# Kernel tuning notes

Measured on AMD Instinct MI355X. Metric: run time of the kernel, lower is better.

## Reference

```python
import jax, jax.numpy as jnp
import numpy as np

N, E, D_IN, D, L = 50000, 800000, 128, 256, 3
BN_EPS = 1e-5


def _bn(x, gamma, beta):
    # torch BatchNorm1d training-mode forward: biased batch statistics over node dim
    m = x.mean(axis=0)
    v = x.var(axis=0)  # ddof=0, matches torch normalization
    return gamma * (x - m) * jax.lax.rsqrt(v + BN_EPS) + beta


def setup_inputs() -> dict:
    key = jax.random.key(0)
    ks = jax.random.split(key, 12)
    s_in = 1.0 / np.sqrt(D_IN)
    s_d = 1.0 / np.sqrt(D)
    s_2d = 1.0 / np.sqrt(2 * D)
    return {
        "pre_node_emb": jax.random.normal(ks[0], (1, N, D_IN), jnp.float32),
        "edge_index": jax.random.randint(ks[1], (1, E, 2), 0, N, jnp.int64),
        "W0": jax.random.uniform(ks[2], (D_IN, D), jnp.float32, -s_in, s_in),
        "b0": jax.random.uniform(ks[3], (D,), jnp.float32, -s_in, s_in),
        "W1": jax.random.uniform(ks[4], (L, D, 2 * D), jnp.float32, -s_d, s_d),
        "b1": jax.random.uniform(ks[5], (L, 2 * D), jnp.float32, -s_d, s_d),
        "g1": jnp.ones((L, 2 * D), jnp.float32),
        "beta1": jnp.zeros((L, 2 * D), jnp.float32),
        "W2": jax.random.uniform(ks[6], (L, 2 * D, D), jnp.float32, -s_2d, s_2d),
        "b2": jax.random.uniform(ks[7], (L, D), jnp.float32, -s_2d, s_2d),
        "gf": jnp.ones((L, D), jnp.float32),
        "betaf": jnp.zeros((L, D), jnp.float32),
    }


def reference(pre_node_emb, edge_index, W0, b0, W1, b1, g1, beta1, W2, b2, gf, betaf):
    x = pre_node_emb[0]            # [N, D_IN]
    ei = edge_index[0]             # [E, 2] -> transposed in torch; rows are (src, dst)
    src, dst = ei[:, 0], ei[:, 1]
    x = x @ W0 + b0                # node embedder -> [N, D]
    for l in range(L):
        # GINConv (eps=0): sum-aggregate neighbor messages, then MLP
        agg = jax.ops.segment_sum(x[src], dst, num_segments=N)   # scatter-add
        h = x + agg
        h = h @ W1[l] + b1[l]
        h = _bn(h, g1[l], beta1[l])
        h = jax.nn.relu(h)
        h = h @ W2[l] + b2[l]
        x = _bn(h + x, gf[l], betaf[l])  # residual + outer BatchNorm
    return x
```

## Files before the change

kernel.cpp:

```cpp
#include <hip/hip_runtime.h>

#define MNODES 50000
#define M_PAD  50048
#define NEDGES 800000
#define DIN    128
#define DD     256
#define D2     512
#define NLAYERS 3
#define BN_EPS 1e-5f
#define NREP   16

typedef unsigned short ushort_t;
typedef __bf16 v8bf __attribute__((ext_vector_type(8)));
typedef unsigned short v8us __attribute__((ext_vector_type(8)));
typedef float  v4f  __attribute__((ext_vector_type(4)));

#define GLOBAL_AS __attribute__((address_space(1)))
#define LDS_AS    __attribute__((address_space(3)))

__device__ __forceinline__ float bf2f(ushort_t u) {
    unsigned x = ((unsigned)u) << 16;
    return __uint_as_float(x);
}
__device__ __forceinline__ ushort_t f2bf(float f) {
    unsigned u = __float_as_uint(f);
    u += 0x7FFF + ((u >> 16) & 1);
    return (ushort_t)(u >> 16);
}
__device__ __forceinline__ void async16(const ushort_t* g, ushort_t* l) {
    __builtin_amdgcn_global_load_lds((const GLOBAL_AS unsigned int*)g,
                                     (LDS_AS unsigned int*)l, 16, 0, 0);
}
#define BARRIER() asm volatile("s_barrier" ::: "memory")
#define VMWAIT8() asm volatile("s_waitcnt vmcnt(8)" ::: "memory")
#define VMWAIT4() asm volatile("s_waitcnt vmcnt(4)" ::: "memory")
#define VMWAIT0() asm volatile("s_waitcnt vmcnt(0)" ::: "memory")
#define LGKM0()   asm volatile("s_waitcnt lgkmcnt(0)" ::: "memory")

#define R0 (M_PAD * DIN)
#define R0V (R0 / 4)
#define RW (DIN * DD + 2 * NLAYERS * DD * D2)
#define NSTATZ (NREP * D2 * 2 + NREP * DD * 2)
__global__ void k_prep_all(const float* __restrict__ pre, ushort_t* __restrict__ preb,
                           const float* __restrict__ W0, const float* __restrict__ W1,
                           const float* __restrict__ W2,
                           ushort_t* __restrict__ W0T, ushort_t* __restrict__ W1T,
                           ushort_t* __restrict__ W2T,
                           float* __restrict__ caf, float* __restrict__ ccf,
                           float* __restrict__ statz, int* __restrict__ deg) {
    int i = blockIdx.x * blockDim.x + threadIdx.x;
    if (i < R0V) {
        int row = i >> 5;
        ushort4 o;
        if (row < MNODES) {
            float4 v = ((const float4*)pre)[i];
            o.x = f2bf(v.x); o.y = f2bf(v.y); o.z = f2bf(v.z); o.w = f2bf(v.w);
        } else {
            o.x = 0; o.y = 0; o.z = 0; o.w = 0;
        }
        ((ushort4*)preb)[i] = o;
        return;
    }
    int j = i - R0V;
    if (j < RW) {
        if (j < DIN * DD) {
            int n = j >> 7, k = j & 127;
            W0T[j] = f2bf(W0[k * DD + n]);
        } else if (j < DIN * DD + NLAYERS * DD * D2) {
            int j2 = j - DIN * DD;
            int l = j2 >> 17, off = j2 & 131071;
            int n = off >> 8, k = off & 255;
            W1T[(size_t)l * 131072 + off] = f2bf(W1[(size_t)l * 131072 + k * D2 + n]);
        } else {
            int j2 = j - DIN * DD - NLAYERS * DD * D2;
            int l = j2 >> 17, off = j2 & 131071;
            int n = off >> 9, k = off & 511;
            W2T[(size_t)l * 131072 + off] = f2bf(W2[(size_t)l * 131072 + k * DD + n]);
        }
        return;
    }
    j -= RW;
    if (j < 256) { caf[j] = 1.f; ccf[j] = 0.f; return; }
    j -= 256;
    if (j < NSTATZ) { statz[j] = 0.f; return; }
    j -= NSTATZ;
    if (j < MNODES) deg[j] = 0;
}

__global__ void k_hist(const int* __restrict__ ei, int* __restrict__ deg) {
    int e = blockIdx.x * blockDim.x + threadIdx.x;
    if (e < NEDGES) atomicAdd(&deg[ei[e * 2 + 1]], 1);
}
__global__ void k_scan1(const int* __restrict__ deg, int* __restrict__ rowptr,
                        int* __restrict__ bsum, int n) {
    __shared__ int tmp[256];
    int tid = threadIdx.x;
    int i = blockIdx.x * 256 + tid;
    int v = (i < n) ? deg[i] : 0;
    tmp[tid] = v;
    __syncthreads();
    #pragma unroll
    for (int off = 1; off < 256; off <<= 1) {
        int t = (tid >= off) ? tmp[tid - off] : 0;
        __syncthreads();
        tmp[tid] += t;
        __syncthreads();
    }
    if (i < n) rowptr[i + 1] = tmp[tid];
    if (tid == 255) bsum[blockIdx.x] = tmp[255];
}
__global__ __launch_bounds__(256)
void k_scan2(int* __restrict__ bsum, int nb) {
    __shared__ int tmp[256];
    int tid = threadIdx.x;
    int v = (tid < nb) ? bsum[tid] : 0;
    tmp[tid] = v;
    __syncthreads();
    #pragma unroll
    for (int off = 1; off < 256; off <<= 1) {
        int t = (tid >= off) ? tmp[tid - off] : 0;
        __syncthreads();
        tmp[tid] += t;
        __syncthreads();
    }
    if (tid < nb) bsum[tid] = tmp[tid] - v;
}
__global__ void k_scan3(const int* __restrict__ deg, const int* __restrict__ bsum,
                        int* __restrict__ rowptr, int* __restrict__ cursor, int n) {
    int i = blockIdx.x * 256 + threadIdx.x;
    if (i == 0) rowptr[0] = 0;
    if (i < n) {
        int incl = rowptr[i + 1] + bsum[i >> 8];
        rowptr[i + 1] = incl;
        cursor[i] = incl - deg[i];
    }
}
__global__ void k_fill(const int* __restrict__ ei, int* __restrict__ cursor,
                       int* __restrict__ col) {
    int e = blockIdx.x * blockDim.x + threadIdx.x;
    if (e < NEDGES) {
        int pos = atomicAdd(&cursor[ei[e * 2 + 1]], 1);
        col[pos] = ei[e * 2];
    }
}

__global__ void k_gather(const int* __restrict__ rowptr, const int* __restrict__ col,
                         const ushort_t* __restrict__ x, const float* __restrict__ ca,
                         const float* __restrict__ cc, ushort_t* __restrict__ out) {
    int node = blockIdx.x * 4 + (threadIdx.x >> 6);
    int lane = threadIdx.x & 63;
    if (node >= MNODES) return;
    const ushort4* xp = (const ushort4*)x;
    ushort4 v = xp[(size_t)node * 64 + lane];
    float a0 = bf2f(v.x), a1 = bf2f(v.y), a2 = bf2f(v.z), a3 = bf2f(v.w);
    int s = rowptr[node], e = rowptr[node + 1];
    int i = s;
    for (; i + 7 < e; i += 8) {
        ushort4 u[8];
        #pragma unroll
        for (int j = 0; j < 8; j++) u[j] = xp[(size_t)col[i + j] * 64 + lane];
        #pragma unroll
        for (int j = 0; j < 8; j++) {
            a0 += bf2f(u[j].x); a1 += bf2f(u[j].y);
            a2 += bf2f(u[j].z); a3 += bf2f(u[j].w);
        }
    }
    for (; i < e; i++) {
        ushort4 u = xp[(size_t)col[i] * 64 + lane];
        a0 += bf2f(u.x); a1 += bf2f(u.y); a2 += bf2f(u.z); a3 += bf2f(u.w);
    }
    int c = lane * 4;
    float dn = (float)(e - s) + 1.0f;
    ushort4 o;
    o.x = f2bf(ca[c + 0] * a0 + dn * cc[c + 0]);
    o.y = f2bf(ca[c + 1] * a1 + dn * cc[c + 1]);
    o.z = f2bf(ca[c + 2] * a2 + dn * cc[c + 2]);
    o.w = f2bf(ca[c + 3] * a3 + dn * cc[c + 3]);
    ((ushort4*)out)[(size_t)node * 64 + lane] = o;
}

__global__ void k_coeffs(float* __restrict__ sums, float* __restrict__ sumsq,
                         const float* __restrict__ g, const float* __restrict__ beta,
                         float* __restrict__ ca, float* __restrict__ cc,
                         float2* __restrict__ cacc, int n) {
    int c = blockIdx.x * blockDim.x + threadIdx.x;
    if (c >= n) return;
    float s = 0.f, q = 0.f;
    #pragma unroll
    for (int r = 0; r < NREP; r++) {
        s += sums[r * n + c];  sums[r * n + c]  = 0.f;
        q += sumsq[r * n + c]; sumsq[r * n + c] = 0.f;
    }
    float mean = s * (1.0f / MNODES);
    float var  = q * (1.0f / MNODES) - mean * mean;
    float a    = g[c] * rsqrtf(var + BN_EPS);
    float b    = beta[c] - a * mean;
    ca[c] = a;
    cc[c] = b;
    if (cacc) cacc[c] = make_float2(a, b);
}

__global__ void k_apply_out(const ushort_t* __restrict__ h, const float* __restrict__ ca,
                            const float* __restrict__ cc, float* __restrict__ out) {
    int i = blockIdx.x * blockDim.x + threadIdx.x;
    if (i >= MNODES * 64) return;
    int c = (i & 63) * 4;
    ushort4 v = ((const ushort4*)h)[i];
    float4 o;
    o.x = ca[c + 0] * bf2f(v.x) + cc[c + 0];
    o.y = ca[c + 1] * bf2f(v.y) + cc[c + 1];
    o.z = ca[c + 2] * bf2f(v.z) + cc[c + 2];
    o.w = ca[c + 3] * bf2f(v.w) + cc[c + 3];
    ((float4*)out)[i] = o;
}

#define LOADA(buf, st)                                                        \
    { buf[0] = *(const v8bf*)(Ap + (st) * 32);                                \
      buf[1] = *(const v8bf*)(Ap + 16 * KT + (st) * 32); }

template<int DO_STATS, int RES, int FUSE_BN, int KT>
__global__ __launch_bounds__(256, 3)
void k_gemm_bf(const ushort_t* __restrict__ A, const ushort_t* __restrict__ WT,
               const float* __restrict__ bias,
               const ushort_t* resid, const float* __restrict__ r_ca,
               const float* __restrict__ r_cc, const float2* __restrict__ cacc,
               ushort_t* out, float* __restrict__ sums, float* __restrict__ sumsq,
               int M, int N) {
    static_assert(KT % 128 == 0, "KT multiple of 128");
    constexpr int nk  = KT >> 5;
    constexpr int nc2 = KT >> 6;
    __shared__ __align__(16) ushort_t Bs[2][128 * 64];
    const int tid = threadIdx.x;
    const int w = tid >> 6, lane = tid & 63;
    const int quad = lane >> 4, l15 = lane & 15;

    const int nxb = N >> 7;
    const int nwg = nxb * (int)gridDim.y;
    const int orig = (int)blockIdx.y * nxb + (int)blockIdx.x;
    const int qq = nwg >> 3, rr = nwg & 7, xc = orig & 7, oi = orig >> 3;
    const int swz = (xc < rr ? xc * (qq + 1) : rr * (qq + 1) + (xc - rr) * qq) + oi;
    const int bx = swz & (nxb - 1);
    const int by = (nxb == 4) ? (swz >> 2) : (swz >> 1);
    const int m0 = by * 128, n0 = bx * 128;

    float2* cacc_lds = nullptr;
    if constexpr (FUSE_BN != 0) {
        __shared__ __align__(16) float2 cacc_s[KT];
        cacc_lds = cacc_s;
        #pragma unroll
        for (int k2 = tid; k2 < KT; k2 += 256) cacc_lds[k2] = cacc[k2];
    }

    const ushort_t* srcB[4];
    {
        int r8 = lane >> 3, s8 = lane & 7;
        #pragma unroll
        for (int j = 0; j < 4; j++) {
            int rowb = (w * 4 + j) * 8 + r8;
            int g = s8 ^ (rowb & 7);
            srcB[j] = WT + (size_t)(n0 + rowb) * KT + g * 8;
        }
    }

    const ushort_t* Ap = A + (size_t)(m0 + w * 32 + l15) * KT + quad * 8;

    v4f acc[2][8];
    #pragma unroll
    for (int i = 0; i < 2; i++)
        #pragma unroll
        for (int j = 0; j < 8; j++)
            acc[i][j] = (v4f){0.f, 0.f, 0.f, 0.f};

    v8bf a0[2], a1[2], a2[2], a3[2];
    LOADA(a0, 0) LOADA(a1, 1) LOADA(a2, 2) LOADA(a3, 3)

    #pragma unroll
    for (int j = 0; j < 4; j++) async16(srcB[j], &Bs[0][(w * 4 + j) * 512]);
    #pragma unroll
    for (int j = 0; j < 4; j++) async16(srcB[j] + 64, &Bs[1][(w * 4 + j) * 512]);
    if constexpr (FUSE_BN != 0) { LGKM0(); }
    VMWAIT4();
    BARRIER();

    #pragma unroll
    for (int c = 0; c < nc2; c++) {
        if (c > 0) {
            BARRIER();
            if (c + 1 < nc2) {
                #pragma unroll
                for (int j = 0; j < 4; j++)
                    async16(srcB[j] + (c + 1) * 64, &Bs[(c + 1) & 1][(w * 4 + j) * 512]);
                VMWAIT8();
            } else {
                VMWAIT0();
            }
            BARRIER();
        }
        const ushort_t* Bb = Bs[c & 1];
        #pragma unroll
        for (int tc = 0; tc < 2; tc++) {
            const int s = c * 2 + tc;
            const int sl4 = s & 3;
            v8bf aUse[2];
            if (sl4 == 0)      { aUse[0] = a0[0]; aUse[1] = a0[1]; }
            else if (sl4 == 1) { aUse[0] = a1[0]; aUse[1] = a1[1]; }
            else if (sl4 == 2) { aUse[0] = a2[0]; aUse[1] = a2[1]; }
            else               { aUse[0] = a3[0]; aUse[1] = a3[1]; }
            if (s + 4 < nk) {
                if (sl4 == 0)      { LOADA(a0, s + 4) }
                else if (sl4 == 1) { LOADA(a1, s + 4) }
                else if (sl4 == 2) { LOADA(a2, s + 4) }
                else               { LOADA(a3, s + 4) }
            }
            if constexpr (FUSE_BN != 0) {
                const float* cb = (const float*)&cacc_lds[(s << 5) + (quad << 3)];
                #pragma unroll
                for (int mt = 0; mt < 2; mt++) {
                    v8us au = *(v8us*)&aUse[mt];
                    v8bf o;
                    #pragma unroll
                    for (int j = 0; j < 8; j++) {
                        float h = bf2f(au[j]);
                        o[j] = (__bf16)fmaxf(fmaf(cb[2 * j], h, cb[2 * j + 1]), 0.f);
                    }
                    aUse[mt] = o;
                }
            }
            v8bf bb0[4];
            #pragma unroll
            for (int nt = 0; nt < 4; nt++) {
                int n_l = nt * 16 + l15;
                int slot = (tc * 4 + quad) ^ (n_l & 7);
                bb0[nt] = *(const v8bf*)&Bb[n_l * 64 + slot * 8];
            }
            #pragma unroll
            for (int mt = 0; mt < 2; mt++)
                #pragma unroll
                for (int nt = 0; nt < 4; nt++)
                    acc[mt][nt] = __builtin_amdgcn_mfma_f32_16x16x32_bf16(
                        aUse[mt], bb0[nt], acc[mt][nt], 0, 0, 0);
            v8bf bb1[4];
            #pragma unroll
            for (int nt = 0; nt < 4; nt++) {
                int n_l = (nt + 4) * 16 + l15;
                int slot = (tc * 4 + quad) ^ (n_l & 7);
                bb1[nt] = *(const v8bf*)&Bb[n_l * 64 + slot * 8];
            }
            #pragma unroll
            for (int mt = 0; mt < 2; mt++)
                #pragma unroll
                for (int nt = 0; nt < 4; nt++)
                    acc[mt][nt + 4] = __builtin_amdgcn_mfma_f32_16x16x32_bf16(
                        aUse[mt], bb1[nt], acc[mt][nt + 4], 0, 0, 0);
        }
    }

    const int mlim = M - m0;
    float s_sum[8], s_sq[8];
    #pragma unroll
    for (int nt = 0; nt < 8; nt++) { s_sum[nt] = 0.f; s_sq[nt] = 0.f; }
    #pragma unroll
    for (int nt = 0; nt < 8; nt++) {
        int colg = n0 + nt * 16 + l15;
        float bia = bias[colg];
        float rca = 0.f, rcc = 0.f;
        if (RES) { rca = r_ca[colg]; rcc = r_cc[colg]; }
        #pragma unroll
        for (int mt = 0; mt < 2; mt++) {
            int rbase = w * 32 + mt * 16 + quad * 4;
            #pragma unroll
            for (int r = 0; r < 4; r++) {
                int rl = rbase + r;
                if (rl < mlim) {
                    size_t idx = (size_t)(m0 + rl) * N + colg;
                    float v = acc[mt][nt][r] + bia;
                    if (RES) v += rca * bf2f(resid[idx]) + rcc;
                    out[idx] = f2bf(v);
                    if (DO_STATS) { s_sum[nt] += v; s_sq[nt] += v * v; }
                }
            }
        }
    }
    if (DO_STATS) {
        const int rep = (by * 4 + w) & (NREP - 1);
        #pragma unroll
        for (int nt = 0; nt < 8; nt++) {
            float s = s_sum[nt], q = s_sq[nt];
            s += __shfl_xor(s, 16); q += __shfl_xor(q, 16);
            s += __shfl_xor(s, 32); q += __shfl_xor(q, 32);
            if (quad == 0) {
                int colg = n0 + nt * 16 + l15;
                atomicAdd(&sums[rep * N + colg], s);
                atomicAdd(&sumsq[rep * N + colg], q);
            }
        }
    }
}

extern "C" void kernel_launch(void* const* d_in, const int* in_sizes, int n_in,
                              void* d_out, int out_size, void* d_ws, size_t ws_size,
                              hipStream_t stream) {
    const float* pre   = (const float*)d_in[0];
    const int*   ei    = (const int*)d_in[1];
    const float* W0    = (const float*)d_in[2];
    const float* b0    = (const float*)d_in[3];
    const float* W1    = (const float*)d_in[4];
    const float* b1    = (const float*)d_in[5];
    const float* g1    = (const float*)d_in[6];
    const float* beta1 = (const float*)d_in[7];
    const float* W2    = (const float*)d_in[8];
    const float* b2    = (const float*)d_in[9];
    const float* gf    = (const float*)d_in[10];
    const float* betaf = (const float*)d_in[11];

    char* p = (char*)d_ws;
    ushort_t* preb = (ushort_t*)p; p += (size_t)M_PAD * DIN * 2;
    ushort_t* ACT1 = (ushort_t*)p; p += (size_t)M_PAD * DD * 2;
    ushort_t* ACT2 = (ushort_t*)p; p += (size_t)M_PAD * DD * 2;
    ushort_t* H1   = (ushort_t*)p; p += (size_t)M_PAD * D2 * 2;
    ushort_t* W0T  = (ushort_t*)p; p += (size_t)DIN * DD * 2;
    ushort_t* W1T  = (ushort_t*)p; p += (size_t)NLAYERS * DD * D2 * 2;
    ushort_t* W2T  = (ushort_t*)p; p += (size_t)NLAYERS * D2 * DD * 2;
    float* sums1  = (float*)p; p += (size_t)NREP * D2 * 4;
    float* sumsq1 = (float*)p; p += (size_t)NREP * D2 * 4;
    float* sumsF  = (float*)p; p += (size_t)NREP * DD * 4;
    float* sumsqF = (float*)p; p += (size_t)NREP * DD * 4;
    float* ca1    = (float*)p; p += D2 * 4;
    float* cc1    = (float*)p; p += D2 * 4;
    float* caf    = (float*)p; p += DD * 4;
    float* ccf    = (float*)p; p += DD * 4;
    float2* cacc1 = (float2*)p; p += D2 * 8;
    int* deg    = (int*)p; p += (size_t)MNODES * 4;
    int* rowptr = (int*)p; p += (size_t)(MNODES + 1) * 4;
    int* cursor = (int*)p; p += (size_t)MNODES * 4;
    int* colx   = (int*)p; p += (size_t)NEDGES * 4;
    int* bsum   = (int*)p; p += 256 * 4;

    dim3 blk(256);
    const int mb = (MNODES + 127) / 128;
    const int nsb = (MNODES + 255) / 256;

    const int prep_total = R0V + RW + 256 + NSTATZ + MNODES;
    k_prep_all<<<(prep_total + 255) / 256, blk, 0, stream>>>(
        pre, preb, W0, W1, W2, W0T, W1T, W2T, caf, ccf, sums1, deg);

    k_hist<<<(NEDGES + 255) / 256, blk, 0, stream>>>(ei, deg);
    k_scan1<<<nsb, blk, 0, stream>>>(deg, rowptr, bsum, MNODES);
    k_scan2<<<1, blk, 0, stream>>>(bsum, nsb);
    k_scan3<<<nsb, blk, 0, stream>>>(deg, bsum, rowptr, cursor, MNODES);
    k_fill<<<(NEDGES + 255) / 256, blk, 0, stream>>>(ei, cursor, colx);

    k_gemm_bf<0, 0, 0, DIN><<<dim3(DD / 128, mb), blk, 0, stream>>>(
        preb, W0T, b0, nullptr, nullptr, nullptr, nullptr,
        ACT2, nullptr, nullptr, MNODES, DD);

    for (int l = 0; l < NLAYERS; l++) {
        k_gather<<<(MNODES + 3) / 4, blk, 0, stream>>>(rowptr, colx, ACT2, caf, ccf, ACT1);

        k_gemm_bf<1, 0, 0, DD><<<dim3(D2 / 128, mb), blk, 0, stream>>>(
            ACT1, W1T + (size_t)l * DD * D2, b1 + (size_t)l * D2,
            nullptr, nullptr, nullptr, nullptr,
            H1, sums1, sumsq1, MNODES, D2);
        k_coeffs<<<2, blk, 0, stream>>>(sums1, sumsq1, g1 + (size_t)l * D2,
                                        beta1 + (size_t)l * D2, ca1, cc1, cacc1, D2);

        k_gemm_bf<1, 1, 1, D2><<<dim3(DD / 128, mb), blk, 0, stream>>>(
            H1, W2T + (size_t)l * D2 * DD, b2 + (size_t)l * DD,
            ACT2, caf, ccf, cacc1,
            ACT2, sumsF, sumsqF, MNODES, DD);
        k_coeffs<<<1, blk, 0, stream>>>(sumsF, sumsqF, gf + (size_t)l * DD,
                                        betaf + (size_t)l * DD, caf, ccf, nullptr, DD);
    }

    k_apply_out<<<(MNODES * 64 + 255) / 256, blk, 0, stream>>>(ACT2, caf, ccf, (float*)d_out);
}
```

Baseline: 750.1 us.

## Split gather across feature slices and transpose weights via LDS tiles

The neighbor gather now assigns 8 lanes per node per 64-byte feature slice, with a second grid dimension of 8 feature partitions. Each wave therefore handles 8 nodes instead of one, which raises the number of independent edges in flight and balances work across nodes with uneven degree. Row reads become 64-byte segments instead of full 512-byte rows, so sector efficiency may drop. Weight transposition also moves out of the prep kernel into a separate LDS-tiled kernel, replacing strided uncoalesced reads with coalesced ones.

```diff
diff --git a/kernel.cpp b/kernel.cpp
--- a/kernel.cpp
+++ b/kernel.cpp
@@ -39,13 +39,8 @@
 
 #define R0 (M_PAD * DIN)
 #define R0V (R0 / 4)
-#define RW (DIN * DD + 2 * NLAYERS * DD * D2)
 #define NSTATZ (NREP * D2 * 2 + NREP * DD * 2)
 __global__ void k_prep_all(const float* __restrict__ pre, ushort_t* __restrict__ preb,
-                           const float* __restrict__ W0, const float* __restrict__ W1,
-                           const float* __restrict__ W2,
-                           ushort_t* __restrict__ W0T, ushort_t* __restrict__ W1T,
-                           ushort_t* __restrict__ W2T,
                            float* __restrict__ caf, float* __restrict__ ccf,
                            float* __restrict__ statz, int* __restrict__ deg) {
     int i = blockIdx.x * blockDim.x + threadIdx.x;
@@ -62,29 +57,41 @@
         return;
     }
     int j = i - R0V;
-    if (j < RW) {
-        if (j < DIN * DD) {
-            int n = j >> 7, k = j & 127;
-            W0T[j] = f2bf(W0[k * DD + n]);
-        } else if (j < DIN * DD + NLAYERS * DD * D2) {
-            int j2 = j - DIN * DD;
-            int l = j2 >> 17, off = j2 & 131071;
-            int n = off >> 8, k = off & 255;
-            W1T[(size_t)l * 131072 + off] = f2bf(W1[(size_t)l * 131072 + k * D2 + n]);
-        } else {
-            int j2 = j - DIN * DD - NLAYERS * DD * D2;
-            int l = j2 >> 17, off = j2 & 131071;
-            int n = off >> 9, k = off & 511;
-            W2T[(size_t)l * 131072 + off] = f2bf(W2[(size_t)l * 131072 + k * DD + n]);
-        }
-        return;
-    }
-    j -= RW;
     if (j < 256) { caf[j] = 1.f; ccf[j] = 0.f; return; }
     j -= 256;
     if (j < NSTATZ) { statz[j] = 0.f; return; }
     j -= NSTATZ;
     if (j < MNODES) deg[j] = 0;
+}
+
+__global__ __launch_bounds__(256)
+void k_wtrans(const float* __restrict__ W0, const float* __restrict__ W1,
+              const float* __restrict__ W2, ushort_t* __restrict__ W0T,
+              ushort_t* __restrict__ W1T, ushort_t* __restrict__ W2T) {
+    __shared__ float tl[32][33];
+    int tile = blockIdx.x;
+    const float* src; ushort_t* dst; int K, N;
+    if (tile < 32) {
+        src = W0; dst = W0T; K = DIN; N = DD;
+    } else if (tile < 416) {
+        int t2 = tile - 32, l = t2 >> 7; t2 &= 127;
+        src = W1 + (size_t)l * DD * D2; dst = W1T + (size_t)l * DD * D2;
+        K = DD; N = D2; tile = t2;
+    } else {
+        int t2 = tile - 416, l = t2 >> 7; t2 &= 127;
+        src = W2 + (size_t)l * D2 * DD; dst = W2T + (size_t)l * D2 * DD;
+        K = D2; N = DD; tile = t2;
+    }
+    int ntn = N >> 5;
+    int kt = tile / ntn, nt = tile - kt * ntn;
+    int tx = threadIdx.x & 31, ty = threadIdx.x >> 5;
+    #pragma unroll
+    for (int r = 0; r < 4; r++)
+        tl[ty + 8 * r][tx] = src[(size_t)(kt * 32 + ty + 8 * r) * N + nt * 32 + tx];
+    __syncthreads();
+    #pragma unroll
+    for (int r = 0; r < 4; r++)
+        dst[(size_t)(nt * 32 + ty + 8 * r) * K + kt * 32 + tx] = f2bf(tl[tx][ty + 8 * r]);
 }
 
 __global__ void k_hist(const int* __restrict__ ei, int* __restrict__ deg) {
@@ -144,39 +151,44 @@
     }
 }
 
-__global__ void k_gather(const int* __restrict__ rowptr, const int* __restrict__ col,
-                         const ushort_t* __restrict__ x, const float* __restrict__ ca,
-                         const float* __restrict__ cc, ushort_t* __restrict__ out) {
-    int node = blockIdx.x * 4 + (threadIdx.x >> 6);
-    int lane = threadIdx.x & 63;
+__global__ __launch_bounds__(256)
+void k_gather(const int* __restrict__ rowptr, const int* __restrict__ col,
+              const ushort_t* __restrict__ x, const float* __restrict__ ca,
+              const float* __restrict__ cc, ushort_t* __restrict__ out) {
+    const int w = threadIdx.x >> 6, lane = threadIdx.x & 63;
+    const int g = lane >> 3, sl = lane & 7;
+    const int node = blockIdx.x * 32 + w * 8 + g;
+    const int p = blockIdx.y;
     if (node >= MNODES) return;
     const ushort4* xp = (const ushort4*)x;
-    ushort4 v = xp[(size_t)node * 64 + lane];
+    const int fo = p * 8 + sl;
+    ushort4 v = xp[(size_t)node * 64 + fo];
     float a0 = bf2f(v.x), a1 = bf2f(v.y), a2 = bf2f(v.z), a3 = bf2f(v.w);
-    int s = rowptr[node], e = rowptr[node + 1];
+    const int s = rowptr[node], e = rowptr[node + 1];
     int i = s;
-    for (; i + 7 < e; i += 8) {
-        ushort4 u[8];
-        #pragma unroll
-        for (int j = 0; j < 8; j++) u[j] = xp[(size_t)col[i + j] * 64 + lane];
-        #pragma unroll
-        for (int j = 0; j < 8; j++) {
-            a0 += bf2f(u[j].x); a1 += bf2f(u[j].y);
-            a2 += bf2f(u[j].z); a3 += bf2f(u[j].w);
-        }
+    for (; i + 3 < e; i += 4) {
+        int c0 = col[i], c1 = col[i + 1], c2 = col[i + 2], c3 = col[i + 3];
+        ushort4 u0 = xp[(size_t)c0 * 64 + fo];
+        ushort4 u1 = xp[(size_t)c1 * 64 + fo];
+        ushort4 u2 = xp[(size_t)c2 * 64 + fo];
+        ushort4 u3 = xp[(size_t)c3 * 64 + fo];
+        a0 += bf2f(u0.x) + bf2f(u1.x) + bf2f(u2.x) + bf2f(u3.x);
+        a1 += bf2f(u0.y) + bf2f(u1.y) + bf2f(u2.y) + bf2f(u3.y);
+        a2 += bf2f(u0.z) + bf2f(u1.z) + bf2f(u2.z) + bf2f(u3.z);
+        a3 += bf2f(u0.w) + bf2f(u1.w) + bf2f(u2.w) + bf2f(u3.w);
     }
     for (; i < e; i++) {
-        ushort4 u = xp[(size_t)col[i] * 64 + lane];
+        ushort4 u = xp[(size_t)col[i] * 64 + fo];
         a0 += bf2f(u.x); a1 += bf2f(u.y); a2 += bf2f(u.z); a3 += bf2f(u.w);
     }
-    int c = lane * 4;
+    const int c = p * 32 + sl * 4;
     float dn = (float)(e - s) + 1.0f;
     ushort4 o;
     o.x = f2bf(ca[c + 0] * a0 + dn * cc[c + 0]);
     o.y = f2bf(ca[c + 1] * a1 + dn * cc[c + 1]);
     o.z = f2bf(ca[c + 2] * a2 + dn * cc[c + 2]);
     o.w = f2bf(ca[c + 3] * a3 + dn * cc[c + 3]);
-    ((ushort4*)out)[(size_t)node * 64 + lane] = o;
+    ((ushort4*)out)[(size_t)node * 64 + fo] = o;
 }
 
 __global__ void k_coeffs(float* __restrict__ sums, float* __restrict__ sumsq,
@@ -440,9 +452,10 @@
     const int mb = (MNODES + 127) / 128;
     const int nsb = (MNODES + 255) / 256;
 
-    const int prep_total = R0V + RW + 256 + NSTATZ + MNODES;
+    const int prep_total = R0V + 256 + NSTATZ + MNODES;
     k_prep_all<<<(prep_total + 255) / 256, blk, 0, stream>>>(
-        pre, preb, W0, W1, W2, W0T, W1T, W2T, caf, ccf, sums1, deg);
+        pre, preb, caf, ccf, sums1, deg);
+    k_wtrans<<<800, blk, 0, stream>>>(W0, W1, W2, W0T, W1T, W2T);
 
     k_hist<<<(NEDGES + 255) / 256, blk, 0, stream>>>(ei, deg);
     k_scan1<<<nsb, blk, 0, stream>>>(deg, rowptr, bsum, MNODES);
@@ -454,8 +467,9 @@
         preb, W0T, b0, nullptr, nullptr, nullptr, nullptr,
         ACT2, nullptr, nullptr, MNODES, DD);
 
+    const int gb = (MNODES + 31) / 32;
     for (int l = 0; l < NLAYERS; l++) {
-        k_gather<<<(MNODES + 3) / 4, blk, 0, stream>>>(rowptr, colx, ACT2, caf, ccf, ACT1);
+        k_gather<<<dim3(gb, 8), blk, 0, stream>>>(rowptr, colx, ACT2, caf, ccf, ACT1);
 
         k_gemm_bf<1, 0, 0, DD><<<dim3(D2 / 128, mb), blk, 0, stream>>>(
             ACT1, W1T + (size_t)l * DD * D2, b1 + (size_t)l * D2,
```

Result: slower. 815.0 us (+8.7%).
